# Performance work log

Measured on AMD Instinct MI355X. Metric: run time of the kernel, lower is better.

Reference implementation:

```python
import jax, jax.numpy as jnp
import numpy as np

EPS = 1e-12  # torch F.normalize default eps


def setup_inputs() -> dict:
    key = jax.random.key(0)
    k1, k2, k3, k4, k5 = jax.random.split(key, 5)
    N, E, D_IN, D_OUT = 100000, 1600000, 128, 128
    features = jax.random.normal(k1, (N, D_IN), dtype=jnp.float32)
    W = jax.random.normal(k2, (D_OUT, D_IN), dtype=jnp.float32) * 0.05
    b = jax.random.normal(k3, (D_OUT,), dtype=jnp.float32) * 0.05
    src = jax.random.randint(k4, (E,), 0, N, dtype=jnp.int32)
    dst = jax.random.randint(k5, (E,), 0, N, dtype=jnp.int32)
    return {"features": features, "W": W, "b": b, "src": src, "dst": dst}


def reference(features, W, b, src, dst):
    N = features.shape[0]
    # sum of features over each node's neighbors: scatter-add messages to dst
    neigh_sum = jax.ops.segment_sum(features[src], dst, num_segments=N)  # [N, D]
    total = jnp.sum(features, axis=0)  # [D]
    # non-neighbor sum (excl. self) + self feature == total - neighbor_sum
    h_NN = total[None, :] - neigh_sum  # [N, D]
    # row-wise L2 normalize (torch F.normalize dim=1)
    norm = jnp.sqrt(jnp.sum(h_NN * h_NN, axis=1, keepdims=True))
    h_norm = h_NN / jnp.maximum(norm, EPS)
    # linear: x @ W.T + b
    return h_norm @ W.T + b
```

## Files before the change

kernel.cpp:

```cpp
#include <hip/hip_runtime.h>
#include <hip/hip_bf16.h>

#define D 128

typedef __bf16 bf16_t;
typedef bf16_t bf16x8 __attribute__((ext_vector_type(8)));
typedef float  f32x4  __attribute__((ext_vector_type(4)));

__device__ __forceinline__ void atomAddF(float* p, float v) {
    unsafeAtomicAdd(p, v);
}

__global__ __launch_bounds__(256) void cvt_colsum_kernel(const float* __restrict__ feat,
                                                         bf16_t* __restrict__ featb,
                                                         float* __restrict__ total,
                                                         long long n8) {
    __shared__ float red[4][16][8];
    int tid = threadIdx.x, lane = tid & 63, w = tid >> 6;
    long long G = (long long)gridDim.x * 256;
    float acc[8];
    #pragma unroll
    for (int e = 0; e < 8; ++e) acc[e] = 0.f;
    for (long long i = (long long)blockIdx.x * 256 + tid; i < n8; i += G) {
        const float4 a = *(const float4*)&feat[i * 8];
        const float4 b = *(const float4*)&feat[i * 8 + 4];
        bf16x8 o;
        o[0] = (bf16_t)a.x; o[1] = (bf16_t)a.y; o[2] = (bf16_t)a.z; o[3] = (bf16_t)a.w;
        o[4] = (bf16_t)b.x; o[5] = (bf16_t)b.y; o[6] = (bf16_t)b.z; o[7] = (bf16_t)b.w;
        *(bf16x8*)&featb[i * 8] = o;
        acc[0] += a.x; acc[1] += a.y; acc[2] += a.z; acc[3] += a.w;
        acc[4] += b.x; acc[5] += b.y; acc[6] += b.z; acc[7] += b.w;
    }
    #pragma unroll
    for (int e = 0; e < 8; ++e) {
        acc[e] += __shfl_xor(acc[e], 16, 64);
        acc[e] += __shfl_xor(acc[e], 32, 64);
    }
    if (lane < 16) {
        #pragma unroll
        for (int e = 0; e < 8; ++e) red[w][lane][e] = acc[e];
    }
    __syncthreads();
    if (tid < 128) {
        int cb = tid >> 3, e = tid & 7;
        float s = red[0][cb][e] + red[1][cb][e] + red[2][cb][e] + red[3][cb][e];
        atomAddF(&total[cb * 8 + e], s);
    }
}

__global__ __launch_bounds__(256) void bucket_count_kernel(const int* __restrict__ dst,
                                                           int* __restrict__ bcount,
                                                           int nE, int NB, int chunk) {
    __shared__ int hist[1024];
    int tid = threadIdx.x;
    int c0 = blockIdx.x * chunk;
    int c1 = c0 + chunk; if (c1 > nE) c1 = nE;
    for (int i = tid; i < NB; i += 256) hist[i] = 0;
    __syncthreads();
    for (int i = c0 + tid; i < c1; i += 256) atomicAdd(&hist[dst[i] >> 8], 1);
    __syncthreads();
    for (int i = tid; i < NB; i += 256) {
        int h = hist[i];
        if (h) atomicAdd(&bcount[i], h);
    }
}

__global__ __launch_bounds__(1024) void bscan_kernel(const int* __restrict__ bcount,
                                                     int* __restrict__ bbase,
                                                     int* __restrict__ bcur,
                                                     int NB, int nE) {
    int tid = threadIdx.x, lane = tid & 63, w = tid >> 6;
    int v = (tid < NB) ? bcount[tid] : 0;
    int x = v;
    #pragma unroll
    for (int off = 1; off < 64; off <<= 1) {
        int y = __shfl_up(x, off, 64);
        if (lane >= off) x += y;
    }
    __shared__ int ws[16];
    if (lane == 63) ws[w] = x;
    __syncthreads();
    if (w == 0 && lane < 16) {
        int s = ws[lane];
        #pragma unroll
        for (int off = 1; off < 16; off <<= 1) {
            int y = __shfl_up(s, off, 64);
            if (lane >= off) s += y;
        }
        ws[lane] = s;
    }
    __syncthreads();
    int base = (w == 0) ? 0 : ws[w - 1];
    int excl = base + x - v;
    if (tid < NB) { bbase[tid] = excl; bcur[tid] = excl; }
    if (tid == 0) bbase[NB] = nE;
}

__global__ __launch_bounds__(256) void bucket_scatter_kernel(const int* __restrict__ src,
                                                             const int* __restrict__ dst,
                                                             int* __restrict__ bcur,
                                                             unsigned* __restrict__ packed,
                                                             int nE, int NB, int chunk) {
    __shared__ int hist[1024];
    __shared__ int cur[1024];
    int tid = threadIdx.x;
    int c0 = blockIdx.x * chunk;
    int c1 = c0 + chunk; if (c1 > nE) c1 = nE;
    for (int i = tid; i < NB; i += 256) hist[i] = 0;
    __syncthreads();
    for (int i = c0 + tid; i < c1; i += 256) atomicAdd(&hist[dst[i] >> 8], 1);
    __syncthreads();
    for (int i = tid; i < NB; i += 256) {
        int h = hist[i];
        cur[i] = h ? atomicAdd(&bcur[i], h) : 0;
    }
    __syncthreads();
    for (int i = c0 + tid; i < c1; i += 256) {
        int t = dst[i];
        int b = t >> 8;
        int off = atomicAdd(&cur[b], 1);
        packed[off] = ((unsigned)(t & 255) << 17) | (unsigned)src[i];
    }
}

__global__ __launch_bounds__(256) void fill_sort_kernel(const unsigned* __restrict__ packed,
                                                        const int* __restrict__ bbase,
                                                        int* __restrict__ ptr,
                                                        int* __restrict__ adj,
                                                        int n, int NB, int nE) {
    __shared__ int cnt[256];
    __shared__ int lcur[256];
    __shared__ int wsum[4];
    int b = blockIdx.x;
    int tid = threadIdx.x, lane = tid & 63, w = tid >> 6;
    int base = bbase[b], end = bbase[b + 1];
    cnt[tid] = 0;
    __syncthreads();
    for (int i = base + tid; i < end; i += 256)
        atomicAdd(&cnt[packed[i] >> 17], 1);
    __syncthreads();
    int v = cnt[tid];
    int x = v;
    #pragma unroll
    for (int off = 1; off < 64; off <<= 1) {
        int y = __shfl_up(x, off, 64);
        if (lane >= off) x += y;
    }
    if (lane == 63) wsum[w] = x;
    __syncthreads();
    int wb = 0;
    for (int k = 0; k < w; ++k) wb += wsum[k];
    int excl = wb + x - v;
    int start = base + excl;
    lcur[tid] = start;
    int node = b * 256 + tid;
    if (node < n) ptr[node] = start;
    if (b == NB - 1 && tid == 0) ptr[n] = nE;
    __syncthreads();
    for (int i = base + tid; i < end; i += 256) {
        unsigned pv = packed[i];
        int j = (int)(pv >> 17);
        int pos = atomicAdd(&lcur[j], 1);
        adj[pos] = (int)(pv & 0x1FFFFu);
    }
}

__global__ __launch_bounds__(256, 4) void gather_mfma_kernel(const bf16_t* __restrict__ featb,
                                                             const int* __restrict__ ptr,
                                                             const int* __restrict__ adj,
                                                             const float* __restrict__ total,
                                                             const float* __restrict__ W,
                                                             const float* __restrict__ bias,
                                                             float* __restrict__ out,
                                                             int n, int ngroups) {
    __shared__ int    s_adj[1024];
    __shared__ bf16_t s_hn[16][136];

    int tid  = threadIdx.x;
    int lane = tid & 63;
    int w    = tid >> 6;
    int quad = lane >> 4;
    int l16  = lane & 15;

    int n0 = w * 32;
    bf16x8 bfrag[4][2];
    #pragma unroll
    for (int s = 0; s < 4; ++s)
        #pragma unroll
        for (int c = 0; c < 2; ++c) {
            const float* wp = W + (size_t)(n0 + 16 * c + l16) * D + 32 * s + 8 * quad;
            float4 wa = *(const float4*)wp;
            float4 wb = *(const float4*)(wp + 4);
            bf16x8 bf;
            bf[0] = (bf16_t)wa.x; bf[1] = (bf16_t)wa.y; bf[2] = (bf16_t)wa.z; bf[3] = (bf16_t)wa.w;
            bf[4] = (bf16_t)wb.x; bf[5] = (bf16_t)wb.y; bf[6] = (bf16_t)wb.z; bf[7] = (bf16_t)wb.w;
            bfrag[s][c] = bf;
        }
    float bias0 = bias[n0 + l16];
    float bias1 = bias[n0 + 16 + l16];

    int k_node = tid >> 4;
    int d8 = (tid & 15) * 8;
    float tot8[8];
    {
        float4 ta = *(const float4*)&total[d8];
        float4 tb = *(const float4*)&total[d8 + 4];
        tot8[0] = ta.x; tot8[1] = ta.y; tot8[2] = ta.z; tot8[3] = ta.w;
        tot8[4] = tb.x; tot8[5] = tb.y; tot8[6] = tb.z; tot8[7] = tb.w;
    }

    for (int g = blockIdx.x; g < ngroups; g += gridDim.x) {
        int v0 = g * 16;
        int v  = v0 + k_node;
        bool valid = v < n;
        int p0 = valid ? ptr[v] : 0;
        int p1 = valid ? ptr[v + 1] : 0;
        int vend = v0 + 16 < n ? v0 + 16 : n;
        int P0 = ptr[v0];
        int P1 = ptr[vend];

        float acc8[8];
        #pragma unroll
        for (int e = 0; e < 8; ++e) acc8[e] = 0.f;

        for (int base = P0; base < P1; base += 1024) {
            int cnt = P1 - base; if (cnt > 1024) cnt = 1024;
            __syncthreads();
            for (int i = tid; i < cnt; i += 256) s_adj[i] = adj[base + i];
            __syncthreads();
            int lo = p0 > base ? p0 : base;
            int hi = p1 < base + cnt ? p1 : base + cnt;
            int p = lo;
            for (; p + 3 < hi; p += 4) {
                int s0 = s_adj[p - base],     s1 = s_adj[p - base + 1];
                int s2 = s_adj[p - base + 2], s3 = s_adj[p - base + 3];
                bf16x8 f0 = *(const bf16x8*)(featb + (size_t)s0 * D + d8);
                bf16x8 f1 = *(const bf16x8*)(featb + (size_t)s1 * D + d8);
                bf16x8 f2 = *(const bf16x8*)(featb + (size_t)s2 * D + d8);
                bf16x8 f3 = *(const bf16x8*)(featb + (size_t)s3 * D + d8);
                #pragma unroll
                for (int e = 0; e < 8; ++e)
                    acc8[e] += ((float)f0[e] + (float)f1[e]) + ((float)f2[e] + (float)f3[e]);
            }
            for (; p < hi; ++p) {
                int s0 = s_adj[p - base];
                bf16x8 f0 = *(const bf16x8*)(featb + (size_t)s0 * D + d8);
                #pragma unroll
                for (int e = 0; e < 8; ++e) acc8[e] += (float)f0[e];
            }
        }

        float h8[8], ss = 0.f;
        #pragma unroll
        for (int e = 0; e < 8; ++e) {
            h8[e] = valid ? (tot8[e] - acc8[e]) : 0.f;
            ss = fmaf(h8[e], h8[e], ss);
        }
        ss += __shfl_xor(ss, 1, 64);
        ss += __shfl_xor(ss, 2, 64);
        ss += __shfl_xor(ss, 4, 64);
        ss += __shfl_xor(ss, 8, 64);
        float rinv = 1.0f / fmaxf(sqrtf(ss), 1e-12f);

        bf16x8 hv;
        #pragma unroll
        for (int e = 0; e < 8; ++e) hv[e] = (bf16_t)(h8[e] * rinv);
        *(bf16x8*)&s_hn[k_node][d8] = hv;
        __syncthreads();

        f32x4 acc0 = {0.f, 0.f, 0.f, 0.f};
        f32x4 acc1 = {0.f, 0.f, 0.f, 0.f};
        #pragma unroll
        for (int s = 0; s < 4; ++s) {
            bf16x8 a = *(const bf16x8*)&s_hn[l16][32 * s + 8 * quad];
            acc0 = __builtin_amdgcn_mfma_f32_16x16x32_bf16(a, bfrag[s][0], acc0, 0, 0, 0);
            acc1 = __builtin_amdgcn_mfma_f32_16x16x32_bf16(a, bfrag[s][1], acc1, 0, 0, 0);
        }
        #pragma unroll
        for (int r = 0; r < 4; ++r) {
            int row = quad * 4 + r;
            int vr = v0 + row;
            if (vr < n) {
                out[(size_t)vr * D + n0 + l16]      = acc0[r] + bias0;
                out[(size_t)vr * D + n0 + 16 + l16] = acc1[r] + bias1;
            }
        }
        __syncthreads();
    }
}

__global__ __launch_bounds__(128) void col_sum_kernel(const float* __restrict__ feat,
                                                      float* __restrict__ total, int n) {
    int d = threadIdx.x;
    float acc = 0.f;
    for (int r = blockIdx.x; r < n; r += gridDim.x)
        acc += feat[(size_t)r * D + d];
    atomAddF(&total[d], acc);
}

__global__ __launch_bounds__(256) void scatter_kernel(const float* __restrict__ feat,
                                                      const int* __restrict__ src,
                                                      const int* __restrict__ dst,
                                                      float* __restrict__ neigh, int nE) {
    long long nwork = (long long)nE * 64;
    long long stride = (long long)gridDim.x * 256;
    for (long long i = (long long)blockIdx.x * 256 + threadIdx.x; i < nwork; i += stride) {
        int e = (int)(i >> 6);
        int d2 = (int)(i & 63) * 2;
        int s = src[e], t = dst[e];
        const float2 vv = *(const float2*)&feat[(size_t)s * D + d2];
        float* p = &neigh[(size_t)t * D + d2];
        atomAddF(p + 0, vv.x);
        atomAddF(p + 1, vv.y);
    }
}

__global__ __launch_bounds__(256) void finalize_kernel(const float* __restrict__ neigh,
                                                       const float* __restrict__ total,
                                                       const float* __restrict__ W,
                                                       const float* __restrict__ bias,
                                                       float* __restrict__ out,
                                                       int n, int ngroups) {
    __shared__ __hip_bfloat16 Wt[D * D];
    __shared__ __align__(16) float hnt[2][D][4];
    __shared__ float red[2][2][4];
    int tid = threadIdx.x;
    for (int idx = tid; idx < D * D; idx += 256) {
        int j = idx & 127, dd = idx >> 7;
        Wt[idx] = __float2bfloat16(W[(size_t)j * D + dd]);
    }
    int half = tid >> 7, d = tid & 127, wih = (tid >> 6) & 1, lane = tid & 63;
    float bj = bias[d], tot = total[d];
    __syncthreads();
    for (int g = blockIdx.x; g < ngroups; g += gridDim.x) {
        int nb = g * 8 + half * 4;
        float h0=0,h1=0,h2=0,h3=0;
        if (nb+0 < n) h0 = tot - neigh[(size_t)(nb+0)*D + d];
        if (nb+1 < n) h1 = tot - neigh[(size_t)(nb+1)*D + d];
        if (nb+2 < n) h2 = tot - neigh[(size_t)(nb+2)*D + d];
        if (nb+3 < n) h3 = tot - neigh[(size_t)(nb+3)*D + d];
        float s0=h0*h0,s1=h1*h1,s2=h2*h2,s3=h3*h3;
        #pragma unroll
        for (int off = 32; off > 0; off >>= 1) {
            s0 += __shfl_xor(s0, off, 64); s1 += __shfl_xor(s1, off, 64);
            s2 += __shfl_xor(s2, off, 64); s3 += __shfl_xor(s3, off, 64);
        }
        if (lane == 0) { red[half][wih][0]=s0; red[half][wih][1]=s1; red[half][wih][2]=s2; red[half][wih][3]=s3; }
        __syncthreads();
        float rinv[4];
        #pragma unroll
        for (int k = 0; k < 4; ++k)
            rinv[k] = 1.0f / fmaxf(sqrtf(red[half][0][k] + red[half][1][k]), 1e-12f);
        hnt[half][d][0]=h0*rinv[0]; hnt[half][d][1]=h1*rinv[1];
        hnt[half][d][2]=h2*rinv[2]; hnt[half][d][3]=h3*rinv[3];
        __syncthreads();
        float a0=0,a1=0,a2=0,a3=0;
        #pragma unroll 8
        for (int dd = 0; dd < D; ++dd) {
            float4 hn4 = *(const float4*)&hnt[half][dd][0];
            float wv = __bfloat162float(Wt[dd * D + d]);
            a0 = fmaf(hn4.x, wv, a0); a1 = fmaf(hn4.y, wv, a1);
            a2 = fmaf(hn4.z, wv, a2); a3 = fmaf(hn4.w, wv, a3);
        }
        if (nb+0 < n) out[(size_t)(nb+0)*D + d] = a0 + bj;
        if (nb+1 < n) out[(size_t)(nb+1)*D + d] = a1 + bj;
        if (nb+2 < n) out[(size_t)(nb+2)*D + d] = a2 + bj;
        if (nb+3 < n) out[(size_t)(nb+3)*D + d] = a3 + bj;
        __syncthreads();
    }
}

static inline size_t align_up(size_t x, size_t a) { return (x + a - 1) & ~(a - 1); }

extern "C" void kernel_launch(void* const* d_in, const int* in_sizes, int n_in,
                              void* d_out, int out_size, void* d_ws, size_t ws_size,
                              hipStream_t stream) {
    const float* feat = (const float*)d_in[0];
    const float* W    = (const float*)d_in[1];
    const float* bias = (const float*)d_in[2];
    const int*   src  = (const int*)d_in[3];
    const int*   dst  = (const int*)d_in[4];
    float* out = (float*)d_out;

    int n  = in_sizes[0] / D;
    int nE = in_sizes[3];
    int NB = (n + 255) / 256;

    char* wsb = (char*)d_ws;
    size_t o_total  = 0;
    size_t o_bcount = 512;
    size_t o_bbase  = o_bcount + 4096;
    size_t o_bcur   = o_bbase + 4608;
    size_t o_ptr    = o_bcur + 4096;
    size_t o_adj    = align_up(o_ptr + (size_t)4 * (n + 1), 512);
    size_t o_packed = o_adj + (size_t)4 * nE;
    size_t o_featb  = align_up(o_packed + (size_t)4 * nE, 512);
    size_t needNew  = o_featb + (size_t)n * D * 2;

    float*    total  = (float*)(wsb + o_total);
    int*      bcount = (int*)(wsb + o_bcount);
    int*      bbase  = (int*)(wsb + o_bbase);
    int*      bcur   = (int*)(wsb + o_bcur);
    int*      ptr    = (int*)(wsb + o_ptr);
    int*      adj    = (int*)(wsb + o_adj);
    unsigned* packed = (unsigned*)(wsb + o_packed);
    bf16_t*   featb  = (bf16_t*)(wsb + o_featb);

    long long n8 = (long long)n * (D / 8);
    int ngroups16 = (n + 15) / 16;
    int grid16 = ngroups16 < 2048 ? ngroups16 : 2048;

    bool packOK = (n <= (1 << 17)) && (NB <= 1024);

    if (ws_size >= needNew && packOK) {
        hipMemsetAsync(wsb, 0, o_bbase, stream);
        cvt_colsum_kernel<<<512, 256, 0, stream>>>(feat, featb, total, n8);
        int chunk = (nE + 511) / 512;
        bucket_count_kernel<<<512, 256, 0, stream>>>(dst, bcount, nE, NB, chunk);
        bscan_kernel<<<1, 1024, 0, stream>>>(bcount, bbase, bcur, NB, nE);
        bucket_scatter_kernel<<<512, 256, 0, stream>>>(src, dst, bcur, packed, nE, NB, chunk);
        fill_sort_kernel<<<NB, 256, 0, stream>>>(packed, bbase, ptr, adj, n, NB, nE);
        gather_mfma_kernel<<<grid16, 256, 0, stream>>>(featb, ptr, adj, total, W, bias,
                                                       out, n, ngroups16);
    } else {
        float* neigh = out;
        if (ws_size >= D * sizeof(float))
            hipMemsetAsync(d_ws, 0, D * sizeof(float), stream);
        hipMemsetAsync(neigh, 0, (size_t)out_size * sizeof(float), stream);
        col_sum_kernel<<<512, 128, 0, stream>>>(feat, total, n);
        scatter_kernel<<<16384, 256, 0, stream>>>(feat, src, dst, neigh, nE);
        int ngroups = (n + 7) / 8;
        finalize_kernel<<<2048, 256, 0, stream>>>(neigh, total, W, bias, out, n, ngroups);
    }
}
```

Measured before the change: 252.1 us.

## Fuse bucket counting into convert kernel, widen fill-sort, batch gather loads

```diff
diff --git a/kernel.cpp b/kernel.cpp
--- a/kernel.cpp
+++ b/kernel.cpp
@@ -11,25 +11,34 @@
     unsafeAtomicAdd(p, v);
 }
 
-__global__ __launch_bounds__(256) void cvt_colsum_kernel(const float* __restrict__ feat,
-                                                         bf16_t* __restrict__ featb,
-                                                         float* __restrict__ total,
-                                                         long long n8) {
+__global__ __launch_bounds__(256) void cvt_colsum_count_kernel(const float* __restrict__ feat,
+                                                               bf16_t* __restrict__ featb,
+                                                               float* __restrict__ total,
+                                                               const int* __restrict__ dst,
+                                                               int* __restrict__ bcount,
+                                                               long long n8, int nE, int NB) {
     __shared__ float red[4][16][8];
+    __shared__ int hist[1024];
     int tid = threadIdx.x, lane = tid & 63, w = tid >> 6;
+    for (int i = tid; i < NB; i += 256) hist[i] = 0;
+    __syncthreads();
     long long G = (long long)gridDim.x * 256;
     float acc[8];
     #pragma unroll
     for (int e = 0; e < 8; ++e) acc[e] = 0.f;
-    for (long long i = (long long)blockIdx.x * 256 + tid; i < n8; i += G) {
-        const float4 a = *(const float4*)&feat[i * 8];
-        const float4 b = *(const float4*)&feat[i * 8 + 4];
-        bf16x8 o;
-        o[0] = (bf16_t)a.x; o[1] = (bf16_t)a.y; o[2] = (bf16_t)a.z; o[3] = (bf16_t)a.w;
-        o[4] = (bf16_t)b.x; o[5] = (bf16_t)b.y; o[6] = (bf16_t)b.z; o[7] = (bf16_t)b.w;
-        *(bf16x8*)&featb[i * 8] = o;
-        acc[0] += a.x; acc[1] += a.y; acc[2] += a.z; acc[3] += a.w;
-        acc[4] += b.x; acc[5] += b.y; acc[6] += b.z; acc[7] += b.w;
+    long long lim = n8 > (long long)nE ? n8 : (long long)nE;
+    for (long long i = (long long)blockIdx.x * 256 + tid; i < lim; i += G) {
+        if (i < n8) {
+            const float4 a = *(const float4*)&feat[i * 8];
+            const float4 b = *(const float4*)&feat[i * 8 + 4];
+            bf16x8 o;
+            o[0] = (bf16_t)a.x; o[1] = (bf16_t)a.y; o[2] = (bf16_t)a.z; o[3] = (bf16_t)a.w;
+            o[4] = (bf16_t)b.x; o[5] = (bf16_t)b.y; o[6] = (bf16_t)b.z; o[7] = (bf16_t)b.w;
+            *(bf16x8*)&featb[i * 8] = o;
+            acc[0] += a.x; acc[1] += a.y; acc[2] += a.z; acc[3] += a.w;
+            acc[4] += b.x; acc[5] += b.y; acc[6] += b.z; acc[7] += b.w;
+        }
+        if (i < (long long)nE) atomicAdd(&hist[dst[i] >> 8], 1);
     }
     #pragma unroll
     for (int e = 0; e < 8; ++e) {
@@ -46,19 +55,6 @@
         float s = red[0][cb][e] + red[1][cb][e] + red[2][cb][e] + red[3][cb][e];
         atomAddF(&total[cb * 8 + e], s);
     }
-}
-
-__global__ __launch_bounds__(256) void bucket_count_kernel(const int* __restrict__ dst,
-                                                           int* __restrict__ bcount,
-                                                           int nE, int NB, int chunk) {
-    __shared__ int hist[1024];
-    int tid = threadIdx.x;
-    int c0 = blockIdx.x * chunk;
-    int c1 = c0 + chunk; if (c1 > nE) c1 = nE;
-    for (int i = tid; i < NB; i += 256) hist[i] = 0;
-    __syncthreads();
-    for (int i = c0 + tid; i < c1; i += 256) atomicAdd(&hist[dst[i] >> 8], 1);
-    __syncthreads();
     for (int i = tid; i < NB; i += 256) {
         int h = hist[i];
         if (h) atomicAdd(&bcount[i], h);
@@ -123,7 +119,7 @@
     }
 }
 
-__global__ __launch_bounds__(256) void fill_sort_kernel(const unsigned* __restrict__ packed,
+__global__ __launch_bounds__(512) void fill_sort_kernel(const unsigned* __restrict__ packed,
                                                         const int* __restrict__ bbase,
                                                         int* __restrict__ ptr,
                                                         int* __restrict__ adj,
@@ -134,30 +130,35 @@
     int b = blockIdx.x;
     int tid = threadIdx.x, lane = tid & 63, w = tid >> 6;
     int base = bbase[b], end = bbase[b + 1];
-    cnt[tid] = 0;
-    __syncthreads();
-    for (int i = base + tid; i < end; i += 256)
+    if (tid < 256) cnt[tid] = 0;
+    __syncthreads();
+    for (int i = base + tid; i < end; i += 512)
         atomicAdd(&cnt[packed[i] >> 17], 1);
     __syncthreads();
-    int v = cnt[tid];
-    int x = v;
-    #pragma unroll
-    for (int off = 1; off < 64; off <<= 1) {
-        int y = __shfl_up(x, off, 64);
-        if (lane >= off) x += y;
-    }
-    if (lane == 63) wsum[w] = x;
-    __syncthreads();
-    int wb = 0;
-    for (int k = 0; k < w; ++k) wb += wsum[k];
-    int excl = wb + x - v;
-    int start = base + excl;
-    lcur[tid] = start;
-    int node = b * 256 + tid;
-    if (node < n) ptr[node] = start;
+    int v = 0, x = 0;
+    if (tid < 256) {
+        v = cnt[tid];
+        x = v;
+        #pragma unroll
+        for (int off = 1; off < 64; off <<= 1) {
+            int y = __shfl_up(x, off, 64);
+            if (lane >= off) x += y;
+        }
+        if (lane == 63) wsum[w] = x;
+    }
+    __syncthreads();
+    if (tid < 256) {
+        int wb = 0;
+        for (int k = 0; k < w; ++k) wb += wsum[k];
+        int excl = wb + x - v;
+        int start = base + excl;
+        lcur[tid] = start;
+        int node = b * 256 + tid;
+        if (node < n) ptr[node] = start;
+    }
     if (b == NB - 1 && tid == 0) ptr[n] = nE;
     __syncthreads();
-    for (int i = base + tid; i < end; i += 256) {
+    for (int i = base + tid; i < end; i += 512) {
         unsigned pv = packed[i];
         int j = (int)(pv >> 17);
         int pos = atomicAdd(&lcur[j], 1);
@@ -173,7 +174,6 @@
                                                              const float* __restrict__ bias,
                                                              float* __restrict__ out,
                                                              int n, int ngroups) {
-    __shared__ int    s_adj[1024];
     __shared__ bf16_t s_hn[16][136];
 
     int tid  = threadIdx.x;
@@ -209,44 +209,33 @@
         tot8[4] = tb.x; tot8[5] = tb.y; tot8[6] = tb.z; tot8[7] = tb.w;
     }
 
+    const bf16_t* fb = featb + d8;
+
     for (int g = blockIdx.x; g < ngroups; g += gridDim.x) {
-        int v0 = g * 16;
-        int v  = v0 + k_node;
+        int v = g * 16 + k_node;
         bool valid = v < n;
         int p0 = valid ? ptr[v] : 0;
         int p1 = valid ? ptr[v + 1] : 0;
-        int vend = v0 + 16 < n ? v0 + 16 : n;
-        int P0 = ptr[v0];
-        int P1 = ptr[vend];
 
         float acc8[8];
         #pragma unroll
         for (int e = 0; e < 8; ++e) acc8[e] = 0.f;
 
-        for (int base = P0; base < P1; base += 1024) {
-            int cnt = P1 - base; if (cnt > 1024) cnt = 1024;
-            __syncthreads();
-            for (int i = tid; i < cnt; i += 256) s_adj[i] = adj[base + i];
-            __syncthreads();
-            int lo = p0 > base ? p0 : base;
-            int hi = p1 < base + cnt ? p1 : base + cnt;
-            int p = lo;
-            for (; p + 3 < hi; p += 4) {
-                int s0 = s_adj[p - base],     s1 = s_adj[p - base + 1];
-                int s2 = s_adj[p - base + 2], s3 = s_adj[p - base + 3];
-                bf16x8 f0 = *(const bf16x8*)(featb + (size_t)s0 * D + d8);
-                bf16x8 f1 = *(const bf16x8*)(featb + (size_t)s1 * D + d8);
-                bf16x8 f2 = *(const bf16x8*)(featb + (size_t)s2 * D + d8);
-                bf16x8 f3 = *(const bf16x8*)(featb + (size_t)s3 * D + d8);
-                #pragma unroll
-                for (int e = 0; e < 8; ++e)
-                    acc8[e] += ((float)f0[e] + (float)f1[e]) + ((float)f2[e] + (float)f3[e]);
+        for (int p = p0; p < p1; p += 8) {
+            int rem = p1 - p;
+            bf16x8 f[8];
+            #pragma unroll
+            for (int i = 0; i < 8; ++i) {
+                int q = (i < rem) ? (p + i) : (p1 - 1);
+                int s0 = adj[q];
+                f[i] = *(const bf16x8*)(fb + (size_t)s0 * D);
             }
-            for (; p < hi; ++p) {
-                int s0 = s_adj[p - base];
-                bf16x8 f0 = *(const bf16x8*)(featb + (size_t)s0 * D + d8);
-                #pragma unroll
-                for (int e = 0; e < 8; ++e) acc8[e] += (float)f0[e];
+            #pragma unroll
+            for (int i = 0; i < 8; ++i) {
+                if (i < rem) {
+                    #pragma unroll
+                    for (int e = 0; e < 8; ++e) acc8[e] += (float)f[i][e];
+                }
             }
         }
 
@@ -279,7 +268,7 @@
         #pragma unroll
         for (int r = 0; r < 4; ++r) {
             int row = quad * 4 + r;
-            int vr = v0 + row;
+            int vr = g * 16 + row;
             if (vr < n) {
                 out[(size_t)vr * D + n0 + l16]      = acc0[r] + bias0;
                 out[(size_t)vr * D + n0 + 16 + l16] = acc1[r] + bias1;
@@ -414,12 +403,12 @@
 
     if (ws_size >= needNew && packOK) {
         hipMemsetAsync(wsb, 0, o_bbase, stream);
-        cvt_colsum_kernel<<<512, 256, 0, stream>>>(feat, featb, total, n8);
+        cvt_colsum_count_kernel<<<512, 256, 0, stream>>>(feat, featb, total, dst, bcount,
+                                                         n8, nE, NB);
         int chunk = (nE + 511) / 512;
-        bucket_count_kernel<<<512, 256, 0, stream>>>(dst, bcount, nE, NB, chunk);
         bscan_kernel<<<1, 1024, 0, stream>>>(bcount, bbase, bcur, NB, nE);
         bucket_scatter_kernel<<<512, 256, 0, stream>>>(src, dst, bcur, packed, nE, NB, chunk);
-        fill_sort_kernel<<<NB, 256, 0, stream>>>(packed, bbase, ptr, adj, n, NB, nE);
+        fill_sort_kernel<<<NB, 512, 0, stream>>>(packed, bbase, ptr, adj, n, NB, nE);
         gather_mfma_kernel<<<grid16, 256, 0, stream>>>(featb, ptr, adj, total, W, bias,
                                                        out, n, ngroups16);
     } else {
```

Result: faster. 244.2 us (-3.1%).
